# Kernel optimization log

Measured on AMD Instinct MI355X. Metric: run time of the kernel, lower is better.

## Reference

```python
import jax, jax.numpy as jnp
import numpy as np

N_NODES = 8192
SEQ = 256
H = 32  # lstm_hdim == gcn_hdim


def lstm_layer(x, Wih, Whh, bih, bhh, return_seq):
    # x: [B, S, D] -> torch nn.LSTM, gate order i,f,g,o
    B = x.shape[0]
    Hd = Whh.shape[1]
    b = bih + bhh

    def step(carry, xt):
        h, c = carry
        z = xt @ Wih.T + h @ Whh.T + b  # [B, 4H]
        i, f, g, o = jnp.split(z, 4, axis=-1)
        c = jax.nn.sigmoid(f) * c + jax.nn.sigmoid(i) * jnp.tanh(g)
        h = jax.nn.sigmoid(o) * jnp.tanh(c)
        return (h, c), (h if return_seq else None)

    init = (jnp.zeros((B, Hd), x.dtype), jnp.zeros((B, Hd), x.dtype))
    (h_n, _), ys = jax.lax.scan(step, init, jnp.transpose(x, (1, 0, 2)))
    if return_seq:
        ys = jnp.transpose(ys, (1, 0, 2))  # [B, S, H]
    return ys, h_n


def layer_norm(x, g, b, eps=1e-5):
    mu = jnp.mean(x, axis=-1, keepdims=True)
    var = jnp.mean((x - mu) ** 2, axis=-1, keepdims=True)
    return (x - mu) * jax.lax.rsqrt(var + eps) * g + b


def gcn_conv(x, edge_index, edge_weight, W, bias, n_nodes):
    # PyG GCNConv with self-loops (fill 1.0) and symmetric normalization.
    h = x @ W  # transform first (in_dim -> out_dim)
    src, dst = edge_index[0], edge_index[1]
    deg = jax.ops.segment_sum(edge_weight, dst, num_segments=n_nodes) + 1.0  # +1 self loop
    dinv = jnp.where(deg > 0, jax.lax.rsqrt(deg), 0.0)
    norm = dinv[src] * edge_weight * dinv[dst]  # [E]
    agg = jax.ops.segment_sum(norm[:, None] * h[src], dst, num_segments=n_nodes)
    agg = agg + h * (dinv * dinv)[:, None]  # self-loop message
    return agg + bias


def setup_inputs() -> dict:
    key = jax.random.key(0)
    ks = jax.random.split(key, 20)
    s = 0.1
    d = {
        "x": jax.random.normal(ks[0], (N_NODES, SEQ), jnp.float32),
        "edge_weight": jax.random.uniform(ks[1], (262144,), jnp.float32),
        "Wih1": jax.random.normal(ks[2], (4 * H, 1)) * s,
        "Whh1": jax.random.normal(ks[3], (4 * H, H)) * s,
        "bih1": jax.random.normal(ks[4], (4 * H,)) * s,
        "bhh1": jax.random.normal(ks[5], (4 * H,)) * s,
        "ln1_g": jnp.ones((H,), jnp.float32),
        "ln1_b": jnp.zeros((H,), jnp.float32),
        "Wih2": jax.random.normal(ks[6], (4 * H, H)) * s,
        "Whh2": jax.random.normal(ks[7], (4 * H, H)) * s,
        "bih2": jax.random.normal(ks[8], (4 * H,)) * s,
        "bhh2": jax.random.normal(ks[9], (4 * H,)) * s,
        "Wg1": jax.random.normal(ks[10], (H, H)) * s,
        "bg1": jax.random.normal(ks[11], (H,)) * s,
        "Wg2": jax.random.normal(ks[12], (H, H)) * s,
        "bg2": jax.random.normal(ks[13], (H,)) * s,
        "Wfc": jax.random.normal(ks[14], (2, H + 1)) * s,
        "bfc": jax.random.normal(ks[15], (2,)) * s,
        "edge_index": jax.random.randint(ks[16], (2, 262144), 0, N_NODES, jnp.int64 if jax.config.jax_enable_x64 else jnp.int32),
    }
    return d


def reference(x, edge_weight, Wih1, Whh1, bih1, bhh1, ln1_g, ln1_b,
              Wih2, Whh2, bih2, bhh2, Wg1, bg1, Wg2, bg2, Wfc, bfc, edge_index):
    n = x.shape[0]
    xs = x[:, :, None]  # [B, S, 1]
    # Temporal module (batched over all samples; dropout off in eval).
    y1, _ = lstm_layer(xs, Wih1, Whh1, bih1, bhh1, return_seq=True)
    y1 = layer_norm(y1, ln1_g, ln1_b)
    _, h2 = lstm_layer(y1, Wih2, Whh2, bih2, bhh2, return_seq=False)  # [B, H]
    gcn_in = h2  # lstm_out.view(-1, lstm_hdim)
    # Spatial module: 2 GCNConv + ELU (dropout between layers is identity in eval).
    g = jax.nn.elu(gcn_conv(gcn_in, edge_index, edge_weight, Wg1, bg1, n))
    g = jax.nn.elu(gcn_conv(g, edge_index, edge_weight, Wg2, bg2, n))
    feat = jnp.concatenate([gcn_in, jnp.mean(g, axis=1, keepdims=True)], axis=1)  # [B, H+1]
    out = feat @ Wfc.T + bfc
    return jax.nn.log_softmax(out, axis=1)
```

## Files before the change

### kernel.cpp

```cpp
#include <hip/hip_runtime.h>

typedef __attribute__((ext_vector_type(8))) short short8;
typedef __attribute__((ext_vector_type(4))) float float4v;

#define NNODES 8192
#define SEQLEN 256
#define HSTR 40

static __device__ __forceinline__ float bf2f(unsigned short u) {
  union { unsigned u; float f; } v; v.u = ((unsigned)u) << 16; return v.f;
}
static __device__ __forceinline__ unsigned short f2bf(float f) {
  union { float f; unsigned u; } v; v.f = f;
  unsigned r = v.u + 0x7FFFu + ((v.u >> 16) & 1u);
  return (unsigned short)(r >> 16);
}
static __device__ __forceinline__ void splitbf8(const float* v, short8& hi) {
#pragma unroll
  for (int j = 0; j < 8; ++j) hi[j] = (short)f2bf(v[j]);
}
static __device__ __forceinline__ float asf(unsigned u) {
  union { unsigned u; float f; } v; v.u = u; return v.f;
}

static __device__ __forceinline__ float lstm_cell(float zi, float zf, float zg,
                                                  float zo, float& c) {
  float ef = __builtin_amdgcn_exp2f(-zf);
  float ei = __builtin_amdgcn_exp2f(-zi);
  float eg = __builtin_amdgcn_exp2f(fminf(zg + zg, 60.f));
  float fterm = c * __builtin_amdgcn_rcpf(1.f + ef);
  float igt = (eg - 1.f) * __builtin_amdgcn_rcpf((1.f + ei) * (eg + 1.f));
  c = fterm + igt;
  float eo = __builtin_amdgcn_exp2f(-zo);
  float ec = __builtin_amdgcn_exp2f(fminf(2.88539008178f * c, 40.f));
  return (ec - 1.f) * __builtin_amdgcn_rcpf((1.f + eo) * (ec + 1.f));
}

__global__ __launch_bounds__(512, 4)
void lstm_fused(const float* __restrict__ x,
                const float* __restrict__ Wih1, const float* __restrict__ Whh1,
                const float* __restrict__ bih1, const float* __restrict__ bhh1,
                const float* __restrict__ ln_g, const float* __restrict__ ln_b,
                const float* __restrict__ Wih2, const float* __restrict__ Whh2,
                const float* __restrict__ bih2, const float* __restrict__ bhh2,
                const float* __restrict__ Wg1,
                const int* __restrict__ ei, const float* __restrict__ ew,
                unsigned long long* __restrict__ pkc, int E,
                float* __restrict__ h2out, float* __restrict__ hWa)
{
  const int tid = threadIdx.x;
  const int w = tid >> 6;
  const int lane = tid & 63;
  const int c = lane & 15;
  const int q = lane >> 4;
  const int hid = w * 4 + q;
  const int nodeBase = blockIdx.x * 16;
  const float L = 1.44269504089f;

  __shared__ __align__(16) float xlds[16 * 260];
  __shared__ __align__(16) unsigned short h1p[2][16 * HSTR];
  __shared__ __align__(16) unsigned short h2p[2][16 * HSTR];
  __shared__ __align__(16) float wgbuf[32 * 33];
  __shared__ __align__(16) float h2f[16 * 33];

  for (int i = tid; i < 16 * 256; i += 512) {
    int nn = i >> 8, tt = i & 255;
    xlds[nn * 260 + tt] = x[(size_t)(nodeBase + nn) * SEQLEN + tt];
  }
  if (tid < 64) xlds[(tid >> 2) * 260 + 256 + (tid & 3)] = 0.f;
  for (int i = tid; i < 1024; i += 512) wgbuf[(i >> 5) * 33 + (i & 31)] = Wg1[i];

  for (int e = blockIdx.x * 512 + tid; e < E; e += gridDim.x * 512) {
    int d = ei[E + e];
    unsigned long long pay = (1ull << 40) |
        (unsigned long long)(unsigned)(ew[e] * 16777216.f + 0.5f);
    atomicAdd(&pkc[d], pay);
  }

  const int browF = (c & 3) * 32 + w * 4 + (c >> 2);
  short8 Bh1, Bi2, Bh2;
  {
    float v[8];
#pragma unroll
    for (int j = 0; j < 8; ++j) v[j] = L * Whh1[browF * 32 + q * 8 + j];
    splitbf8(v, Bh1);
#pragma unroll
    for (int j = 0; j < 8; ++j) v[j] = L * Wih2[browF * 32 + q * 8 + j] * ln_g[q * 8 + j];
    splitbf8(v, Bi2);
#pragma unroll
    for (int j = 0; j < 8; ++j) v[j] = L * Whh2[browF * 32 + q * 8 + j];
    splitbf8(v, Bh2);
  }

  float Gp[4], C1a[4], C2a[4];
#pragma unroll
  for (int r = 0; r < 4; ++r) {
    const int br = r * 32 + hid;
    float sG = 0.f, sB = 0.f;
    for (int k = 0; k < 32; ++k) {
      float wv = Wih2[br * 32 + k];
      sG += wv * ln_g[k];
      sB += wv * ln_b[k];
    }
    Gp[r] = L * sG;
    C1a[r] = L * (bih1[br] + bhh1[br]);
    C2a[r] = L * (sB + bih2[br] + bhh2[br]);
  }
  const float4v C1 = {C1a[0], C1a[1], C1a[2], C1a[3]};
  const float4v C2 = {C2a[0], C2a[1], C2a[2], C2a[3]};
  const float4v z4 = {0.f, 0.f, 0.f, 0.f};
  float w1v[4];
#pragma unroll
  for (int g = 0; g < 4; ++g) w1v[g] = L * Wih1[g * 32 + hid];

  const int hWr = c * HSTR + hid;
  const int hRd = c * HSTR + q * 8;

  short8 h1A = {0,0,0,0,0,0,0,0};
  short8 h2A = {0,0,0,0,0,0,0,0};
  float c1 = 0.f, c2 = 0.f, hv2 = 0.f;
  __syncthreads();

  {
    float xv = xlds[c * 260 + 0];
    float hv = lstm_cell(fmaf(xv, w1v[0], C1[0]), fmaf(xv, w1v[1], C1[1]),
                         fmaf(xv, w1v[2], C1[2]), fmaf(xv, w1v[3], C1[3]), c1);
    h1p[1][hWr] = f2bf(hv);
  }
  __syncthreads();
  h1A = *(const short8*)&h1p[1][hRd];

  auto step = [&](int t, int pl) {
    float xv = xlds[c * 260 + t + 1];
    float4v Cx = {fmaf(xv, w1v[0], C1[0]), fmaf(xv, w1v[1], C1[1]),
                  fmaf(xv, w1v[2], C1[2]), fmaf(xv, w1v[3], C1[3])};
    float4v za = __builtin_amdgcn_mfma_f32_16x16x32_bf16(Bh1, h1A, Cx, 0, 0, 0);
    float4v db = __builtin_amdgcn_mfma_f32_16x16x32_bf16(Bh2, h2A, C2, 0, 0, 0);

    float s = 0.f, s2 = 0.f;
    {
      const unsigned* hw = (const unsigned*)&h1A;
#pragma unroll
      for (int j = 0; j < 4; ++j) {
        unsigned u = hw[j];
        float flo = asf(u << 16);
        float fhi = asf(u & 0xFFFF0000u);
        s += flo; s2 = fmaf(flo, flo, s2);
        s += fhi; s2 = fmaf(fhi, fhi, s2);
      }
    }
    s  += __shfl_xor(s, 16, 64);  s  += __shfl_xor(s, 32, 64);
    s2 += __shfl_xor(s2, 16, 64); s2 += __shfl_xor(s2, 32, 64);
    float mu = s * (1.f / 32.f);
    float var = s2 * (1.f / 32.f) - mu * mu;
    float rstd = __builtin_amdgcn_rsqf(var + 1e-5f);
    float mur = rstd * mu;

    float4v da = __builtin_amdgcn_mfma_f32_16x16x32_bf16(Bi2, h1A, z4, 0, 0, 0);

    hv2 = lstm_cell(fmaf(rstd, da[0], fmaf(-mur, Gp[0], db[0])),
                    fmaf(rstd, da[1], fmaf(-mur, Gp[1], db[1])),
                    fmaf(rstd, da[2], fmaf(-mur, Gp[2], db[2])),
                    fmaf(rstd, da[3], fmaf(-mur, Gp[3], db[3])), c2);
    float hv = lstm_cell(za[0], za[1], za[2], za[3], c1);

    unsigned pk;
    asm("v_cvt_pk_bf16_f32 %0, %1, %2" : "=v"(pk) : "v"(hv), "v"(hv2));
    h1p[pl][hWr] = (unsigned short)pk;
    h2p[pl][hWr] = (unsigned short)(pk >> 16);

    __syncthreads();
    h1A = *(const short8*)&h1p[pl][hRd];
    h2A = *(const short8*)&h2p[pl][hRd];
  };

  for (int t = 0; t < SEQLEN; t += 2) {
    step(t, 0);
    step(t + 1, 1);
  }

  h2out[(size_t)(nodeBase + c) * 32 + hid] = hv2;

  h2f[c * 33 + hid] = hv2;
  __syncthreads();
  {
    int nl = tid >> 5, j = tid & 31;
    float acc = 0.f;
#pragma unroll
    for (int k = 0; k < 32; ++k) acc = fmaf(h2f[nl * 33 + k], wgbuf[k * 33 + j], acc);
    hWa[(size_t)(nodeBase + nl) * 32 + j] = acc;
  }
}

__global__ __launch_bounds__(1024, 1)
void scan_k(const unsigned long long* __restrict__ pk, int* __restrict__ off,
            int* __restrict__ pos, float* __restrict__ dinv) {
  __shared__ int wtot[16];
  __shared__ int wexcl[16];
  int tid = threadIdx.x;
  int wv = tid >> 6, lane = tid & 63;
  int base = tid * 8;
  int v[8]; int sum = 0;
#pragma unroll
  for (int i = 0; i < 8; ++i) {
    unsigned long long u = pk[base + i];
    v[i] = (int)(u >> 40);
    float degv = (float)(u & 0xFFFFFFFFFFull) * (1.f / 16777216.f);
    dinv[base + i] = rsqrtf(degv + 1.0f);
    sum += v[i];
  }
  int incl = sum;
#pragma unroll
  for (int d = 1; d < 64; d <<= 1) {
    int t = __shfl_up(incl, d, 64);
    if (lane >= d) incl += t;
  }
  if (lane == 63) wtot[wv] = incl;
  __syncthreads();
  if (wv == 0 && lane < 16) {
    int wval = wtot[lane];
    int wincl = wval;
#pragma unroll
    for (int d = 1; d < 16; d <<= 1) {
      int t = __shfl_up(wincl, d, 64);
      if (lane >= d) wincl += t;
    }
    wexcl[lane] = wincl - wval;
  }
  __syncthreads();
  int run = wexcl[wv] + (incl - sum);
#pragma unroll
  for (int i = 0; i < 8; ++i) {
    off[base + i] = run; pos[base + i] = run; run += v[i];
  }
  if (tid == 1023) off[8192] = run;
}

__global__ void scatter_k(const int* __restrict__ ei, const float* __restrict__ ew,
                          const float* __restrict__ dinv, int* __restrict__ pos,
                          int2* __restrict__ ed, int E) {
  int e = blockIdx.x * 256 + threadIdx.x;
  if (e >= E) return;
  int sidx = ei[e], d = ei[E + e];
  int p = atomicAdd(&pos[d], 1);
  int2 pay;
  pay.x = sidx;
  pay.y = __float_as_int(dinv[sidx] * ew[e] * dinv[d]);
  ed[p] = pay;
}

__global__ __launch_bounds__(512, 4)
void gather_mid_k(const int* __restrict__ off, const int2* __restrict__ ed,
                  const float* __restrict__ dinv, const float* __restrict__ hWa,
                  const float* __restrict__ bg1, const float* __restrict__ Wg2,
                  float* __restrict__ aggB) {
  __shared__ float wg[32 * 33];
  __shared__ float g1buf[16][33];
  int tid = threadIdx.x;
  for (int i = tid; i < 1024; i += 512) wg[(i >> 5) * 33 + (i & 31)] = Wg2[i];
  int nl = tid >> 5, j = tid & 31;
  int node = blockIdx.x * 16 + nl;
  float dv = dinv[node];
  float a0 = dv * dv * hWa[(size_t)node * 32 + j];
  float a1 = 0.f, a2 = 0.f, a3 = 0.f;
  int p0 = off[node], p1 = off[node + 1];
  int p = p0;
  for (; p + 3 < p1; p += 4) {
    int2 e0 = ed[p], e1 = ed[p + 1], e2 = ed[p + 2], e3 = ed[p + 3];
    a0 = fmaf(__int_as_float(e0.y), hWa[(size_t)e0.x * 32 + j], a0);
    a1 = fmaf(__int_as_float(e1.y), hWa[(size_t)e1.x * 32 + j], a1);
    a2 = fmaf(__int_as_float(e2.y), hWa[(size_t)e2.x * 32 + j], a2);
    a3 = fmaf(__int_as_float(e3.y), hWa[(size_t)e3.x * 32 + j], a3);
  }
  for (; p < p1; ++p) {
    int2 e0 = ed[p];
    a0 = fmaf(__int_as_float(e0.y), hWa[(size_t)e0.x * 32 + j], a0);
  }
  float v = (a0 + a1) + (a2 + a3) + bg1[j];
  g1buf[nl][j] = (v > 0.f) ? v : expm1f(v);
  __syncthreads();
  float acc = 0.f;
#pragma unroll
  for (int k = 0; k < 32; ++k) acc = fmaf(g1buf[nl][k], wg[k * 33 + j], acc);
  aggB[(size_t)node * 32 + j] = acc;
}

__global__ __launch_bounds__(512, 4)
void gather_final_k(const int* __restrict__ off, const int2* __restrict__ ed,
                    const float* __restrict__ dinv, const float* __restrict__ aggB,
                    const float* __restrict__ bg2, const float* __restrict__ h2o,
                    const float* __restrict__ Wfc, const float* __restrict__ bfc,
                    float* __restrict__ out) {
  int tid = threadIdx.x;
  int nl = tid >> 5, j = tid & 31;
  int node = blockIdx.x * 16 + nl;
  float dv = dinv[node];
  float a0 = dv * dv * aggB[(size_t)node * 32 + j];
  float a1 = 0.f, a2 = 0.f, a3 = 0.f;
  int p0 = off[node], p1 = off[node + 1];
  int p = p0;
  for (; p + 3 < p1; p += 4) {
    int2 e0 = ed[p], e1 = ed[p + 1], e2 = ed[p + 2], e3 = ed[p + 3];
    a0 = fmaf(__int_as_float(e0.y), aggB[(size_t)e0.x * 32 + j], a0);
    a1 = fmaf(__int_as_float(e1.y), aggB[(size_t)e1.x * 32 + j], a1);
    a2 = fmaf(__int_as_float(e2.y), aggB[(size_t)e2.x * 32 + j], a2);
    a3 = fmaf(__int_as_float(e3.y), aggB[(size_t)e3.x * 32 + j], a3);
  }
  for (; p < p1; ++p) {
    int2 e0 = ed[p];
    a0 = fmaf(__int_as_float(e0.y), aggB[(size_t)e0.x * 32 + j], a0);
  }
  float v = (a0 + a1) + (a2 + a3) + bg2[j];
  float e = (v > 0.f) ? v : expm1f(v);
  float h2v = h2o[(size_t)node * 32 + j];
  float p0s = h2v * Wfc[j];
  float p1s = h2v * Wfc[33 + j];
#pragma unroll
  for (int m = 1; m < 32; m <<= 1) {
    e   += __shfl_xor(e, m, 32);
    p0s += __shfl_xor(p0s, m, 32);
    p1s += __shfl_xor(p1s, m, 32);
  }
  if (j == 0) {
    float mean = e * (1.f / 32.f);
    float o0 = p0s + mean * Wfc[32] + bfc[0];
    float o1 = p1s + mean * Wfc[65] + bfc[1];
    float mx = fmaxf(o0, o1);
    float l = mx + logf(expf(o0 - mx) + expf(o1 - mx));
    out[node * 2 + 0] = o0 - l;
    out[node * 2 + 1] = o1 - l;
  }
}

extern "C" void kernel_launch(void* const* d_in, const int* in_sizes, int n_in,
                              void* d_out, int out_size, void* d_ws, size_t ws_size,
                              hipStream_t stream) {
  const float* x    = (const float*)d_in[0];
  const float* ew   = (const float*)d_in[1];
  const float* Wih1 = (const float*)d_in[2];
  const float* Whh1 = (const float*)d_in[3];
  const float* bih1 = (const float*)d_in[4];
  const float* bhh1 = (const float*)d_in[5];
  const float* ln_g = (const float*)d_in[6];
  const float* ln_b = (const float*)d_in[7];
  const float* Wih2 = (const float*)d_in[8];
  const float* Whh2 = (const float*)d_in[9];
  const float* bih2 = (const float*)d_in[10];
  const float* bhh2 = (const float*)d_in[11];
  const float* Wg1  = (const float*)d_in[12];
  const float* bg1  = (const float*)d_in[13];
  const float* Wg2  = (const float*)d_in[14];
  const float* bg2  = (const float*)d_in[15];
  const float* Wfc  = (const float*)d_in[16];
  const float* bfc  = (const float*)d_in[17];
  const int* ei     = (const int*)d_in[18];
  float* out = (float*)d_out;
  const int E = in_sizes[1];

  float* ws   = (float*)d_ws;
  float* h2o  = ws;
  float* hWa  = ws + 262144;
  float* aggB = ws + 524288;
  unsigned long long* pk = (unsigned long long*)(ws + 786432);
  float* dinv = ws + 802816;
  int*   off  = (int*)(ws + 811008);
  int*   pos  = (int*)(ws + 819208);
  int2*  ed   = (int2*)(ws + 827400);

  hipMemsetAsync((void*)pk, 0, 8192 * sizeof(unsigned long long), stream);
  hipLaunchKernelGGL(lstm_fused, dim3(NNODES / 16), dim3(512), 0, stream,
                     x, Wih1, Whh1, bih1, bhh1, ln_g, ln_b,
                     Wih2, Whh2, bih2, bhh2, Wg1, ei, ew, pk, E, h2o, hWa);
  hipLaunchKernelGGL(scan_k, dim3(1), dim3(1024), 0, stream, pk, off, pos, dinv);
  hipLaunchKernelGGL(scatter_k, dim3((E + 255) / 256), dim3(256), 0, stream, ei, ew, dinv, pos, ed, E);
  hipLaunchKernelGGL(gather_mid_k, dim3(NNODES / 16), dim3(512), 0, stream,
                     off, ed, dinv, hWa, bg1, Wg2, aggB);
  hipLaunchKernelGGL(gather_final_k, dim3(NNODES / 16), dim3(512), 0, stream,
                     off, ed, dinv, aggB, bg2, h2o, Wfc, bfc, out);
}
```

Measured before the change: 369.3 us.

## Fuse degree scan into LSTM kernel, MFMA row-sum, paired LSTM cell

Removes the separate single-block scan kernel. Each LSTM block now signals an atomic counter after its degree atomics, and block 0 waits on that counter at the end and performs the prefix scan and dinv computation itself. It also computes the layer-norm sum with an MFMA against a ones vector instead of shuffles, and evaluates both LSTM cells together, sharing reciprocals. The cost is a spin-wait in block 0 that relies on all blocks making progress, plus an extra memset for the counter.

```diff
diff --git a/kernel.cpp b/kernel.cpp
--- a/kernel.cpp
+++ b/kernel.cpp
@@ -2,14 +2,12 @@
 
 typedef __attribute__((ext_vector_type(8))) short short8;
 typedef __attribute__((ext_vector_type(4))) float float4v;
+typedef __attribute__((ext_vector_type(2))) float float2v;
 
 #define NNODES 8192
 #define SEQLEN 256
 #define HSTR 40
 
-static __device__ __forceinline__ float bf2f(unsigned short u) {
-  union { unsigned u; float f; } v; v.u = ((unsigned)u) << 16; return v.f;
-}
 static __device__ __forceinline__ unsigned short f2bf(float f) {
   union { float f; unsigned u; } v; v.f = f;
   unsigned r = v.u + 0x7FFFu + ((v.u >> 16) & 1u);
@@ -36,6 +34,27 @@
   return (ec - 1.f) * __builtin_amdgcn_rcpf((1.f + eo) * (ec + 1.f));
 }
 
+static __device__ __forceinline__ void lstm_cell2(
+    const float4v& z1, const float4v& z2,
+    float2v& cc, float& h1, float& h2) {
+  float2v ef = {__builtin_amdgcn_exp2f(-z1[1]), __builtin_amdgcn_exp2f(-z2[1])};
+  float2v ei = {__builtin_amdgcn_exp2f(-z1[0]), __builtin_amdgcn_exp2f(-z2[0])};
+  float2v eg = {__builtin_amdgcn_exp2f(fminf(z1[2] + z1[2], 60.f)),
+                __builtin_amdgcn_exp2f(fminf(z2[2] + z2[2], 60.f))};
+  float2v A = 1.f + ef;
+  float2v D = (1.f + ei) * (eg + 1.f);
+  float2v AD = A * D;
+  float2v R = {__builtin_amdgcn_rcpf(AD.x), __builtin_amdgcn_rcpf(AD.y)};
+  cc = cc * (D * R) + (eg - 1.f) * (A * R);
+  float2v eo = {__builtin_amdgcn_exp2f(-z1[3]), __builtin_amdgcn_exp2f(-z2[3])};
+  float2v ec = {__builtin_amdgcn_exp2f(fminf(2.88539008178f * cc.x, 40.f)),
+                __builtin_amdgcn_exp2f(fminf(2.88539008178f * cc.y, 40.f))};
+  float2v Q = (1.f + eo) * (ec + 1.f);
+  float RQ = __builtin_amdgcn_rcpf(Q.x * Q.y);
+  h1 = (ec.x - 1.f) * (Q.y * RQ);
+  h2 = (ec.y - 1.f) * (Q.x * RQ);
+}
+
 __global__ __launch_bounds__(512, 4)
 void lstm_fused(const float* __restrict__ x,
                 const float* __restrict__ Wih1, const float* __restrict__ Whh1,
@@ -46,6 +65,9 @@
                 const float* __restrict__ Wg1,
                 const int* __restrict__ ei, const float* __restrict__ ew,
                 unsigned long long* __restrict__ pkc, int E,
+                unsigned* __restrict__ ctr,
+                int* __restrict__ offp, int* __restrict__ posp,
+                float* __restrict__ dinvp,
                 float* __restrict__ h2out, float* __restrict__ hWa)
 {
   const int tid = threadIdx.x;
@@ -62,6 +84,7 @@
   __shared__ __align__(16) unsigned short h2p[2][16 * HSTR];
   __shared__ __align__(16) float wgbuf[32 * 33];
   __shared__ __align__(16) float h2f[16 * 33];
+  __shared__ int scanw[16];
 
   for (int i = tid; i < 16 * 256; i += 512) {
     int nn = i >> 8, tt = i & 255;
@@ -76,6 +99,10 @@
         (unsigned long long)(unsigned)(ew[e] * 16777216.f + 0.5f);
     atomicAdd(&pkc[d], pay);
   }
+  __threadfence();
+  __syncthreads();
+  if (tid == 0)
+    __hip_atomic_fetch_add(ctr, 1u, __ATOMIC_RELEASE, __HIP_MEMORY_SCOPE_AGENT);
 
   const int browF = (c & 3) * 32 + w * 4 + (c >> 2);
   short8 Bh1, Bi2, Bh2;
@@ -91,6 +118,8 @@
     for (int j = 0; j < 8; ++j) v[j] = L * Whh2[browF * 32 + q * 8 + j];
     splitbf8(v, Bh2);
   }
+  const short8 Ones = {0x3F80, 0x3F80, 0x3F80, 0x3F80,
+                       0x3F80, 0x3F80, 0x3F80, 0x3F80};
 
   float Gp[4], C1a[4], C2a[4];
 #pragma unroll
@@ -118,13 +147,16 @@
 
   short8 h1A = {0,0,0,0,0,0,0,0};
   short8 h2A = {0,0,0,0,0,0,0,0};
-  float c1 = 0.f, c2 = 0.f, hv2 = 0.f;
+  float2v cc = {0.f, 0.f};
+  float hv2 = 0.f;
   __syncthreads();
 
   {
+    float c1tmp = 0.f;
     float xv = xlds[c * 260 + 0];
     float hv = lstm_cell(fmaf(xv, w1v[0], C1[0]), fmaf(xv, w1v[1], C1[1]),
-                         fmaf(xv, w1v[2], C1[2]), fmaf(xv, w1v[3], C1[3]), c1);
+                         fmaf(xv, w1v[2], C1[2]), fmaf(xv, w1v[3], C1[3]), c1tmp);
+    cc.x = c1tmp;
     h1p[1][hWr] = f2bf(hv);
   }
   __syncthreads();
@@ -136,33 +168,34 @@
                   fmaf(xv, w1v[2], C1[2]), fmaf(xv, w1v[3], C1[3])};
     float4v za = __builtin_amdgcn_mfma_f32_16x16x32_bf16(Bh1, h1A, Cx, 0, 0, 0);
     float4v db = __builtin_amdgcn_mfma_f32_16x16x32_bf16(Bh2, h2A, C2, 0, 0, 0);
-
-    float s = 0.f, s2 = 0.f;
+    float4v sv = __builtin_amdgcn_mfma_f32_16x16x32_bf16(Ones, h1A, z4, 0, 0, 0);
+
+    float2v s2v = {0.f, 0.f};
     {
       const unsigned* hw = (const unsigned*)&h1A;
 #pragma unroll
       for (int j = 0; j < 4; ++j) {
         unsigned u = hw[j];
-        float flo = asf(u << 16);
-        float fhi = asf(u & 0xFFFF0000u);
-        s += flo; s2 = fmaf(flo, flo, s2);
-        s += fhi; s2 = fmaf(fhi, fhi, s2);
+        float2v p = {asf(u << 16), asf(u & 0xFFFF0000u)};
+        s2v = p * p + s2v;
       }
     }
-    s  += __shfl_xor(s, 16, 64);  s  += __shfl_xor(s, 32, 64);
+    float s2 = s2v.x + s2v.y;
     s2 += __shfl_xor(s2, 16, 64); s2 += __shfl_xor(s2, 32, 64);
-    float mu = s * (1.f / 32.f);
-    float var = s2 * (1.f / 32.f) - mu * mu;
+    float mu = sv[0] * (1.f / 32.f);
+    float var = fmaf(s2, 1.f / 32.f, -mu * mu);
     float rstd = __builtin_amdgcn_rsqf(var + 1e-5f);
     float mur = rstd * mu;
 
     float4v da = __builtin_amdgcn_mfma_f32_16x16x32_bf16(Bi2, h1A, z4, 0, 0, 0);
 
-    hv2 = lstm_cell(fmaf(rstd, da[0], fmaf(-mur, Gp[0], db[0])),
-                    fmaf(rstd, da[1], fmaf(-mur, Gp[1], db[1])),
-                    fmaf(rstd, da[2], fmaf(-mur, Gp[2], db[2])),
-                    fmaf(rstd, da[3], fmaf(-mur, Gp[3], db[3])), c2);
-    float hv = lstm_cell(za[0], za[1], za[2], za[3], c1);
+    float4v z2v = {fmaf(rstd, da[0], fmaf(-mur, Gp[0], db[0])),
+                   fmaf(rstd, da[1], fmaf(-mur, Gp[1], db[1])),
+                   fmaf(rstd, da[2], fmaf(-mur, Gp[2], db[2])),
+                   fmaf(rstd, da[3], fmaf(-mur, Gp[3], db[3]))};
+    float hv, hvb;
+    lstm_cell2(za, z2v, cc, hv, hvb);
+    hv2 = hvb;
 
     unsigned pk;
     asm("v_cvt_pk_bf16_f32 %0, %1, %2" : "=v"(pk) : "v"(hv), "v"(hv2));
@@ -190,50 +223,51 @@
     for (int k = 0; k < 32; ++k) acc = fmaf(h2f[nl * 33 + k], wgbuf[k * 33 + j], acc);
     hWa[(size_t)(nodeBase + nl) * 32 + j] = acc;
   }
-}
-
-__global__ __launch_bounds__(1024, 1)
-void scan_k(const unsigned long long* __restrict__ pk, int* __restrict__ off,
-            int* __restrict__ pos, float* __restrict__ dinv) {
-  __shared__ int wtot[16];
-  __shared__ int wexcl[16];
-  int tid = threadIdx.x;
-  int wv = tid >> 6, lane = tid & 63;
-  int base = tid * 8;
-  int v[8]; int sum = 0;
-#pragma unroll
-  for (int i = 0; i < 8; ++i) {
-    unsigned long long u = pk[base + i];
-    v[i] = (int)(u >> 40);
-    float degv = (float)(u & 0xFFFFFFFFFFull) * (1.f / 16777216.f);
-    dinv[base + i] = rsqrtf(degv + 1.0f);
-    sum += v[i];
-  }
-  int incl = sum;
-#pragma unroll
-  for (int d = 1; d < 64; d <<= 1) {
-    int t = __shfl_up(incl, d, 64);
-    if (lane >= d) incl += t;
-  }
-  if (lane == 63) wtot[wv] = incl;
-  __syncthreads();
-  if (wv == 0 && lane < 16) {
-    int wval = wtot[lane];
-    int wincl = wval;
-#pragma unroll
-    for (int d = 1; d < 16; d <<= 1) {
-      int t = __shfl_up(wincl, d, 64);
-      if (lane >= d) wincl += t;
-    }
-    wexcl[lane] = wincl - wval;
-  }
-  __syncthreads();
-  int run = wexcl[wv] + (incl - sum);
-#pragma unroll
-  for (int i = 0; i < 8; ++i) {
-    off[base + i] = run; pos[base + i] = run; run += v[i];
-  }
-  if (tid == 1023) off[8192] = run;
+
+  if (blockIdx.x == 0) {
+    if (tid == 0) {
+      while (__hip_atomic_load(ctr, __ATOMIC_ACQUIRE,
+                               __HIP_MEMORY_SCOPE_AGENT) < gridDim.x)
+        __builtin_amdgcn_s_sleep(8);
+    }
+    __syncthreads();
+    const int base2 = tid * 16;
+    int v[16]; int sum = 0;
+#pragma unroll
+    for (int i = 0; i < 16; ++i) {
+      unsigned long long u = __hip_atomic_load(&pkc[base2 + i], __ATOMIC_RELAXED,
+                                               __HIP_MEMORY_SCOPE_AGENT);
+      v[i] = (int)(u >> 40);
+      float degv = (float)(u & 0xFFFFFFFFFFull) * (1.f / 16777216.f);
+      dinvp[base2 + i] = rsqrtf(degv + 1.0f);
+      sum += v[i];
+    }
+    int incl = sum;
+#pragma unroll
+    for (int d = 1; d < 64; d <<= 1) {
+      int t = __shfl_up(incl, d, 64);
+      if (lane >= d) incl += t;
+    }
+    if (lane == 63) scanw[w] = incl;
+    __syncthreads();
+    if (w == 0 && lane < 8) {
+      int wval = scanw[lane];
+      int wincl = wval;
+#pragma unroll
+      for (int d = 1; d < 8; d <<= 1) {
+        int t = __shfl_up(wincl, d, 64);
+        if (lane >= d) wincl += t;
+      }
+      scanw[8 + lane] = wincl - wval;
+    }
+    __syncthreads();
+    int run = scanw[8 + w] + (incl - sum);
+#pragma unroll
+    for (int i = 0; i < 16; ++i) {
+      offp[base2 + i] = run; posp[base2 + i] = run; run += v[i];
+    }
+    if (tid == 511) offp[8192] = run;
+  }
 }
 
 __global__ void scatter_k(const int* __restrict__ ei, const float* __restrict__ ew,
@@ -364,14 +398,16 @@
   unsigned long long* pk = (unsigned long long*)(ws + 786432);
   float* dinv = ws + 802816;
   int*   off  = (int*)(ws + 811008);
+  unsigned* ctr = (unsigned*)(ws + 819202);
   int*   pos  = (int*)(ws + 819208);
   int2*  ed   = (int2*)(ws + 827400);
 
   hipMemsetAsync((void*)pk, 0, 8192 * sizeof(unsigned long long), stream);
+  hipMemsetAsync((void*)ctr, 0, sizeof(unsigned), stream);
   hipLaunchKernelGGL(lstm_fused, dim3(NNODES / 16), dim3(512), 0, stream,
                      x, Wih1, Whh1, bih1, bhh1, ln_g, ln_b,
-                     Wih2, Whh2, bih2, bhh2, Wg1, ei, ew, pk, E, h2o, hWa);
-  hipLaunchKernelGGL(scan_k, dim3(1), dim3(1024), 0, stream, pk, off, pos, dinv);
+                     Wih2, Whh2, bih2, bhh2, Wg1, ei, ew, pk, E,
+                     ctr, off, pos, dinv, h2o, hWa);
   hipLaunchKernelGGL(scatter_k, dim3((E + 255) / 256), dim3(256), 0, stream, ei, ew, dinv, pos, ed, E);
   hipLaunchKernelGGL(gather_mid_k, dim3(NNODES / 16), dim3(512), 0, stream,
                      off, ed, dinv, hWa, bg1, Wg2, aggB);
```

Measured after the change: 406.9 us. 1.1x slower.
